# Kernel optimization log

Hardware: AMD Instinct MI355X
Metric: run time of the kernel (lower is better)

Reference implementation:

```python
import jax, jax.numpy as jnp
import numpy as np

B, H, L, D = 2, 8, 512, 64
TEMP = 8.0  # sqrt(D)


def setup_inputs() -> dict:
    key = jax.random.key(0)
    ks = jax.random.split(key, 6)
    q = jax.random.normal(ks[0], (B, H, L, D), jnp.float32)
    k = jax.random.normal(ks[1], (B, H, L, D), jnp.float32)
    v = jax.random.normal(ks[2], (B, H, L, D), jnp.float32)
    adj_k = jax.random.normal(ks[3], (B, L, L, D), jnp.float32)
    adj_v = jax.random.normal(ks[4], (B, L, L, D), jnp.float32)
    mask = jax.random.randint(ks[5], (B, 1, 1, L), 0, 2, jnp.int32)
    return {"q": q, "k": k, "v": v, "adj_k": adj_k, "adj_v": adj_v, "mask": mask}


def reference(q, k, v, adj_k, adj_v, mask):
    qs = q / TEMP
    # standard QK^T term + relation term: score[b,h,i,j] += q[b,h,i]. adj_k[b,i,j]
    attn = jnp.einsum('bhid,bhjd->bhij', qs, k) + jnp.einsum('bhid,bijd->bhij', qs, adj_k)
    attn = jnp.where(mask == 0, jnp.float32(-10000.0), attn)
    attn = jax.nn.softmax(attn, axis=-1)  # dropout p=0 (eval / deterministic)
    # standard AV term + relation term: out[b,h,i] += sum_j attn[b,h,i,j]*adj_v[b,i,j]
    out = jnp.einsum('bhij,bhjd->bhid', attn, v) + jnp.einsum('bhij,bijd->bhid', attn, adj_v)
    return out, attn
```

## Files before the change

kernel.cpp:

```cpp
#include <hip/hip_runtime.h>

constexpr int B  = 2;
constexpr int NH = 8;
constexpr int L  = 512;
constexpr int D  = 64;
constexpr float INV_TEMP = 0.125f;

__global__ __launch_bounds__(256) void k1_qk(const float* __restrict__ q,
                                             const float* __restrict__ k,
                                             float* __restrict__ s1) {
  const int bh = blockIdx.x, it = blockIdx.y, jt = blockIdx.z;
  __shared__ float Qs[64][68];
  __shared__ float Ks[128][68];
  const int t = threadIdx.x;
  const float* qb = q + ((size_t)bh * L + it * 64) * D;
  const float* kb = k + ((size_t)bh * L + jt * 128) * D;
#pragma unroll
  for (int n0 = 0; n0 < 4; ++n0) {
    int n = t + (n0 << 8);
    int r = n >> 4, c = (n & 15) << 2;
    float4 a = *(const float4*)(qb + (size_t)r * D + c);
    a.x *= INV_TEMP; a.y *= INV_TEMP; a.z *= INV_TEMP; a.w *= INV_TEMP;
    *(float4*)&Qs[r][c] = a;
  }
#pragma unroll
  for (int n0 = 0; n0 < 8; ++n0) {
    int n = t + (n0 << 8);
    int r = n >> 4, c = (n & 15) << 2;
    *(float4*)&Ks[r][c] = *(const float4*)(kb + (size_t)r * D + c);
  }
  __syncthreads();
  const int i0 = t >> 4, j0 = t & 15;
  float acc[4][8] = {};
#pragma unroll 1
  for (int kc = 0; kc < 64; kc += 4) {
    float4 a[4], b[8];
#pragma unroll
    for (int m = 0; m < 4; ++m) a[m] = *(const float4*)&Qs[i0 + 16 * m][kc];
#pragma unroll
    for (int n = 0; n < 8; ++n) b[n] = *(const float4*)&Ks[j0 + 16 * n][kc];
#pragma unroll
    for (int m = 0; m < 4; ++m)
#pragma unroll
      for (int n = 0; n < 8; ++n)
        acc[m][n] = fmaf(a[m].x, b[n].x,
                    fmaf(a[m].y, b[n].y,
                    fmaf(a[m].z, b[n].z,
                    fmaf(a[m].w, b[n].w, acc[m][n]))));
  }
  float* sb = s1 + ((size_t)bh * L + it * 64) * L + jt * 128;
#pragma unroll
  for (int m = 0; m < 4; ++m) {
    float* srow = sb + (size_t)(i0 + 16 * m) * L;
#pragma unroll
    for (int n = 0; n < 8; ++n) srow[j0 + 16 * n] = acc[m][n];
  }
}

__global__ __launch_bounds__(512, 8) void k2_fused(
    const float* __restrict__ q, const float* __restrict__ v,
    const float* __restrict__ adj_k, const float* __restrict__ adj_v,
    const int* __restrict__ mask, const float* __restrict__ s1,
    float* __restrict__ out, float* __restrict__ attn) {
  const int b = blockIdx.x >> 9, i = blockIdx.x & (L - 1);
  const int t = threadIdx.x;
  const int lane = t & 63;
  const int w = __builtin_amdgcn_readfirstlane(t >> 6);

  __shared__ float sc[NH][L];
  __shared__ float ak[64][65];

  const float* akb = adj_k + ((size_t)b * L + i) * (size_t)(L * D);
  const float* qh  = q  + (((size_t)b * NH + w) * L + i) * D;
  const float* s1r = s1 + (((size_t)b * NH + w) * L + i) * L;

  const int sr0 = t >> 4, scol = (t & 15) << 2, sr1 = sr0 + 32;
  float4 pf0 = *(const float4*)(akb + (size_t)sr0 * D + scol);
  float4 pf1 = *(const float4*)(akb + (size_t)sr1 * D + scol);

  for (int jc = 0; jc < L; jc += 64) {
    ak[sr0][scol] = pf0.x; ak[sr0][scol + 1] = pf0.y;
    ak[sr0][scol + 2] = pf0.z; ak[sr0][scol + 3] = pf0.w;
    ak[sr1][scol] = pf1.x; ak[sr1][scol + 1] = pf1.y;
    ak[sr1][scol + 2] = pf1.z; ak[sr1][scol + 3] = pf1.w;
    __syncthreads();
    if (jc + 64 < L) {
      const float* nb = akb + (size_t)(jc + 64) * D;
      pf0 = *(const float4*)(nb + (size_t)sr0 * D + scol);
      pf1 = *(const float4*)(nb + (size_t)sr1 * D + scol);
    }
    float acc = 0.f;
#pragma unroll
    for (int dc = 0; dc < D; dc += 4) {
      float4 q4 = *(const float4*)(qh + dc);
      acc = fmaf(q4.x, ak[lane][dc],
            fmaf(q4.y, ak[lane][dc + 1],
            fmaf(q4.z, ak[lane][dc + 2],
            fmaf(q4.w, ak[lane][dc + 3], acc))));
    }
    sc[w][jc + lane] = s1r[jc + lane] + acc * INV_TEMP;
    __syncthreads();
  }

  {
    const int* mrow = mask + b * L;
    float* arow = attn + (((size_t)b * NH + w) * L + i) * L;
    float vals[8];
    float mx = -3.4e38f;
#pragma unroll
    for (int m = 0; m < 8; ++m) {
      int jj = lane + (m << 6);
      float s = sc[w][jj];
      s = (mrow[jj] == 0) ? -10000.0f : s;
      vals[m] = s;
      mx = fmaxf(mx, s);
    }
#pragma unroll
    for (int off = 32; off > 0; off >>= 1) mx = fmaxf(mx, __shfl_xor(mx, off, 64));
    float sum = 0.f;
#pragma unroll
    for (int m = 0; m < 8; ++m) { vals[m] = __expf(vals[m] - mx); sum += vals[m]; }
#pragma unroll
    for (int off = 32; off > 0; off >>= 1) sum += __shfl_xor(sum, off, 64);
    const float inv = 1.0f / sum;
#pragma unroll
    for (int m = 0; m < 8; ++m) {
      int jj = lane + (m << 6);
      float p = vals[m] * inv;
      arow[jj] = p;
      sc[w][jj] = p;
    }
  }
  __syncthreads();

  {
    const int jb = w << 6;
    const float* avp = adj_v + ((size_t)b * L + i) * (size_t)(L * D)
                             + (size_t)jb * D + lane;
    const float* vb  = v + (size_t)b * NH * (size_t)(L * D)
                         + (size_t)jb * D + lane;
    float* opart = &ak[0][0];
#pragma unroll
    for (int g = 0; g < 2; ++g) {
      const int h0 = g * 4;
      float p0 = sc[h0][jb + lane],     p1 = sc[h0 + 1][jb + lane],
            p2 = sc[h0 + 2][jb + lane], p3 = sc[h0 + 3][jb + lane];
      const float* w0 = vb + (size_t)(h0    ) * (L * D);
      const float* w1 = vb + (size_t)(h0 + 1) * (L * D);
      const float* w2 = vb + (size_t)(h0 + 2) * (L * D);
      const float* w3 = vb + (size_t)(h0 + 3) * (L * D);
      float o0 = 0.f, o1 = 0.f, o2 = 0.f, o3 = 0.f;
#pragma unroll 4
      for (int j = 0; j < 64; ++j) {
        float av = avp[(size_t)j * D];
        float x0 = w0[(size_t)j * D];
        float x1 = w1[(size_t)j * D];
        float x2 = w2[(size_t)j * D];
        float x3 = w3[(size_t)j * D];
        float pj0 = __uint_as_float(__builtin_amdgcn_readlane(__float_as_uint(p0), j));
        float pj1 = __uint_as_float(__builtin_amdgcn_readlane(__float_as_uint(p1), j));
        float pj2 = __uint_as_float(__builtin_amdgcn_readlane(__float_as_uint(p2), j));
        float pj3 = __uint_as_float(__builtin_amdgcn_readlane(__float_as_uint(p3), j));
        o0 = fmaf(pj0, av + x0, o0);
        o1 = fmaf(pj1, av + x1, o1);
        o2 = fmaf(pj2, av + x2, o2);
        o3 = fmaf(pj3, av + x3, o3);
      }
      opart[(w << 9) + (h0    ) * 64 + lane] = o0;
      opart[(w << 9) + (h0 + 1) * 64 + lane] = o1;
      opart[(w << 9) + (h0 + 2) * 64 + lane] = o2;
      opart[(w << 9) + (h0 + 3) * 64 + lane] = o3;
    }
    __syncthreads();
    float r = 0.f;
#pragma unroll
    for (int wv = 0; wv < 8; ++wv) r += opart[(wv << 9) + (w << 6) + lane];
    out[(((size_t)b * NH + w) * L + i) * D + lane] = r;
  }
}

extern "C" void kernel_launch(void* const* d_in, const int* in_sizes, int n_in,
                              void* d_out, int out_size, void* d_ws, size_t ws_size,
                              hipStream_t stream) {
  const float* q     = (const float*)d_in[0];
  const float* k     = (const float*)d_in[1];
  const float* v     = (const float*)d_in[2];
  const float* adj_k = (const float*)d_in[3];
  const float* adj_v = (const float*)d_in[4];
  const int*   mask  = (const int*)d_in[5];
  float* out  = (float*)d_out;
  float* attn = out + (size_t)B * NH * L * D;
  float* s1   = (float*)d_ws;

  dim3 g1(B * NH, L / 64, L / 128);
  k1_qk<<<g1, 256, 0, stream>>>(q, k, s1);
  k2_fused<<<B * L, 512, 0, stream>>>(q, v, adj_k, adj_v, mask, s1, out, attn);
}
```

Measured before the change: 346.2 us.

## Split attn·V into separate tiled GEMM kernel and restructure adj_k/adj_v passes

The attn·V term is moved out of the fused per-row kernel into a new tiled GEMM kernel that reads attn back and adds its result into out. The fused kernel now handles only the adj_k score term and the adj_v output term. The adj_k pass reads each adjacency row once into registers and computes all heads together, with no shared-memory staging. The adj_v pass uses float4 loads and a shuffle reduction instead of per-head scalar strided loads of both v and adj_v. The QK kernel tile shrinks to 64x64 for more blocks, at the cost of a third launch and an extra round trip of attn through memory.

```diff
diff --git a/kernel.cpp b/kernel.cpp
--- a/kernel.cpp
+++ b/kernel.cpp
@@ -11,10 +11,10 @@
                                              float* __restrict__ s1) {
   const int bh = blockIdx.x, it = blockIdx.y, jt = blockIdx.z;
   __shared__ float Qs[64][68];
-  __shared__ float Ks[128][68];
+  __shared__ float Ks[64][68];
   const int t = threadIdx.x;
   const float* qb = q + ((size_t)bh * L + it * 64) * D;
-  const float* kb = k + ((size_t)bh * L + jt * 128) * D;
+  const float* kb = k + ((size_t)bh * L + jt * 64) * D;
 #pragma unroll
   for (int n0 = 0; n0 < 4; ++n0) {
     int n = t + (n0 << 8);
@@ -22,96 +22,86 @@
     float4 a = *(const float4*)(qb + (size_t)r * D + c);
     a.x *= INV_TEMP; a.y *= INV_TEMP; a.z *= INV_TEMP; a.w *= INV_TEMP;
     *(float4*)&Qs[r][c] = a;
-  }
-#pragma unroll
-  for (int n0 = 0; n0 < 8; ++n0) {
-    int n = t + (n0 << 8);
-    int r = n >> 4, c = (n & 15) << 2;
     *(float4*)&Ks[r][c] = *(const float4*)(kb + (size_t)r * D + c);
   }
   __syncthreads();
   const int i0 = t >> 4, j0 = t & 15;
-  float acc[4][8] = {};
+  float acc[4][4] = {};
 #pragma unroll 1
   for (int kc = 0; kc < 64; kc += 4) {
-    float4 a[4], b[8];
+    float4 a[4], b[4];
 #pragma unroll
     for (int m = 0; m < 4; ++m) a[m] = *(const float4*)&Qs[i0 + 16 * m][kc];
 #pragma unroll
-    for (int n = 0; n < 8; ++n) b[n] = *(const float4*)&Ks[j0 + 16 * n][kc];
+    for (int n = 0; n < 4; ++n) b[n] = *(const float4*)&Ks[j0 + 16 * n][kc];
 #pragma unroll
     for (int m = 0; m < 4; ++m)
 #pragma unroll
-      for (int n = 0; n < 8; ++n)
+      for (int n = 0; n < 4; ++n)
         acc[m][n] = fmaf(a[m].x, b[n].x,
                     fmaf(a[m].y, b[n].y,
                     fmaf(a[m].z, b[n].z,
                     fmaf(a[m].w, b[n].w, acc[m][n]))));
   }
-  float* sb = s1 + ((size_t)bh * L + it * 64) * L + jt * 128;
+  float* sb = s1 + ((size_t)bh * L + it * 64) * L + jt * 64;
 #pragma unroll
   for (int m = 0; m < 4; ++m) {
     float* srow = sb + (size_t)(i0 + 16 * m) * L;
 #pragma unroll
-    for (int n = 0; n < 8; ++n) srow[j0 + 16 * n] = acc[m][n];
-  }
-}
-
-__global__ __launch_bounds__(512, 8) void k2_fused(
-    const float* __restrict__ q, const float* __restrict__ v,
-    const float* __restrict__ adj_k, const float* __restrict__ adj_v,
-    const int* __restrict__ mask, const float* __restrict__ s1,
-    float* __restrict__ out, float* __restrict__ attn) {
+    for (int n = 0; n < 4; ++n) srow[j0 + 16 * n] = acc[m][n];
+  }
+}
+
+__global__ __launch_bounds__(512, 4) void k2_fused(
+    const float* __restrict__ q, const float* __restrict__ adj_k,
+    const float* __restrict__ adj_v, const int* __restrict__ mask,
+    const float* __restrict__ s1, float* __restrict__ out,
+    float* __restrict__ attn) {
   const int b = blockIdx.x >> 9, i = blockIdx.x & (L - 1);
   const int t = threadIdx.x;
   const int lane = t & 63;
   const int w = __builtin_amdgcn_readfirstlane(t >> 6);
-
+  const int jb = w << 6;
   __shared__ float sc[NH][L];
-  __shared__ float ak[64][65];
-
-  const float* akb = adj_k + ((size_t)b * L + i) * (size_t)(L * D);
-  const float* qh  = q  + (((size_t)b * NH + w) * L + i) * D;
-  const float* s1r = s1 + (((size_t)b * NH + w) * L + i) * L;
-
-  const int sr0 = t >> 4, scol = (t & 15) << 2, sr1 = sr0 + 32;
-  float4 pf0 = *(const float4*)(akb + (size_t)sr0 * D + scol);
-  float4 pf1 = *(const float4*)(akb + (size_t)sr1 * D + scol);
-
-  for (int jc = 0; jc < L; jc += 64) {
-    ak[sr0][scol] = pf0.x; ak[sr0][scol + 1] = pf0.y;
-    ak[sr0][scol + 2] = pf0.z; ak[sr0][scol + 3] = pf0.w;
-    ak[sr1][scol] = pf1.x; ak[sr1][scol + 1] = pf1.y;
-    ak[sr1][scol + 2] = pf1.z; ak[sr1][scol + 3] = pf1.w;
-    __syncthreads();
-    if (jc + 64 < L) {
-      const float* nb = akb + (size_t)(jc + 64) * D;
-      pf0 = *(const float4*)(nb + (size_t)sr0 * D + scol);
-      pf1 = *(const float4*)(nb + (size_t)sr1 * D + scol);
-    }
-    float acc = 0.f;
-#pragma unroll
-    for (int dc = 0; dc < D; dc += 4) {
-      float4 q4 = *(const float4*)(qh + dc);
-      acc = fmaf(q4.x, ak[lane][dc],
-            fmaf(q4.y, ak[lane][dc + 1],
-            fmaf(q4.z, ak[lane][dc + 2],
-            fmaf(q4.w, ak[lane][dc + 3], acc))));
-    }
-    sc[w][jc + lane] = s1r[jc + lane] + acc * INV_TEMP;
-    __syncthreads();
-  }
 
   {
-    const int* mrow = mask + b * L;
+    const float* akr = adj_k + (((size_t)b * L + i) * L + jb + lane) * D;
+    float4 row[16];
+#pragma unroll
+    for (int dc = 0; dc < 16; ++dc) row[dc] = *(const float4*)(akr + 4 * dc);
+    const int mv = mask[b * L + jb + lane];
+    float acc[NH];
+#pragma unroll
+    for (int h = 0; h < NH; ++h) {
+      const float* qh = q + (((size_t)b * NH + h) * L + i) * D;
+      float a0 = 0.f, a1 = 0.f;
+#pragma unroll
+      for (int dc = 0; dc < 16; dc += 2) {
+        float4 q4 = *(const float4*)(qh + 4 * dc);
+        float4 q5 = *(const float4*)(qh + 4 * dc + 4);
+        a0 = fmaf(q4.x, row[dc].x, fmaf(q4.y, row[dc].y,
+             fmaf(q4.z, row[dc].z, fmaf(q4.w, row[dc].w, a0))));
+        a1 = fmaf(q5.x, row[dc + 1].x, fmaf(q5.y, row[dc + 1].y,
+             fmaf(q5.z, row[dc + 1].z, fmaf(q5.w, row[dc + 1].w, a1))));
+      }
+      acc[h] = a0 + a1;
+    }
+#pragma unroll
+    for (int h = 0; h < NH; ++h) {
+      float s = s1[(((size_t)b * NH + h) * L + i) * L + jb + lane]
+                + acc[h] * INV_TEMP;
+      sc[h][jb + lane] = (mv == 0) ? -10000.0f : s;
+    }
+  }
+  __syncthreads();
+
+  {
     float* arow = attn + (((size_t)b * NH + w) * L + i) * L;
     float vals[8];
     float mx = -3.4e38f;
 #pragma unroll
     for (int m = 0; m < 8; ++m) {
-      int jj = lane + (m << 6);
-      float s = sc[w][jj];
-      s = (mrow[jj] == 0) ? -10000.0f : s;
+      float s = sc[w][lane + (m << 6)];
       vals[m] = s;
       mx = fmaxf(mx, s);
     }
@@ -134,49 +124,104 @@
   __syncthreads();
 
   {
-    const int jb = w << 6;
-    const float* avp = adj_v + ((size_t)b * L + i) * (size_t)(L * D)
-                             + (size_t)jb * D + lane;
-    const float* vb  = v + (size_t)b * NH * (size_t)(L * D)
-                         + (size_t)jb * D + lane;
-    float* opart = &ak[0][0];
-#pragma unroll
-    for (int g = 0; g < 2; ++g) {
-      const int h0 = g * 4;
-      float p0 = sc[h0][jb + lane],     p1 = sc[h0 + 1][jb + lane],
-            p2 = sc[h0 + 2][jb + lane], p3 = sc[h0 + 3][jb + lane];
-      const float* w0 = vb + (size_t)(h0    ) * (L * D);
-      const float* w1 = vb + (size_t)(h0 + 1) * (L * D);
-      const float* w2 = vb + (size_t)(h0 + 2) * (L * D);
-      const float* w3 = vb + (size_t)(h0 + 3) * (L * D);
-      float o0 = 0.f, o1 = 0.f, o2 = 0.f, o3 = 0.f;
+    const int js = lane >> 4, dq = lane & 15;
+    const float* avb = adj_v + ((size_t)b * L + i) * (size_t)(L * D)
+                             + (size_t)jb * D + 4 * dq;
+    float4 o[NH];
+#pragma unroll
+    for (int h = 0; h < NH; ++h) o[h] = make_float4(0.f, 0.f, 0.f, 0.f);
 #pragma unroll 4
-      for (int j = 0; j < 64; ++j) {
-        float av = avp[(size_t)j * D];
-        float x0 = w0[(size_t)j * D];
-        float x1 = w1[(size_t)j * D];
-        float x2 = w2[(size_t)j * D];
-        float x3 = w3[(size_t)j * D];
-        float pj0 = __uint_as_float(__builtin_amdgcn_readlane(__float_as_uint(p0), j));
-        float pj1 = __uint_as_float(__builtin_amdgcn_readlane(__float_as_uint(p1), j));
-        float pj2 = __uint_as_float(__builtin_amdgcn_readlane(__float_as_uint(p2), j));
-        float pj3 = __uint_as_float(__builtin_amdgcn_readlane(__float_as_uint(p3), j));
-        o0 = fmaf(pj0, av + x0, o0);
-        o1 = fmaf(pj1, av + x1, o1);
-        o2 = fmaf(pj2, av + x2, o2);
-        o3 = fmaf(pj3, av + x3, o3);
+    for (int jj = 0; jj < 64; jj += 4) {
+      const float4 av = *(const float4*)(avb + (size_t)(jj + js) * D);
+      const int j = jb + jj + js;
+#pragma unroll
+      for (int h = 0; h < NH; ++h) {
+        float p = sc[h][j];
+        o[h].x = fmaf(p, av.x, o[h].x);
+        o[h].y = fmaf(p, av.y, o[h].y);
+        o[h].z = fmaf(p, av.z, o[h].z);
+        o[h].w = fmaf(p, av.w, o[h].w);
       }
-      opart[(w << 9) + (h0    ) * 64 + lane] = o0;
-      opart[(w << 9) + (h0 + 1) * 64 + lane] = o1;
-      opart[(w << 9) + (h0 + 2) * 64 + lane] = o2;
-      opart[(w << 9) + (h0 + 3) * 64 + lane] = o3;
+    }
+#pragma unroll
+    for (int h = 0; h < NH; ++h) {
+      o[h].x += __shfl_xor(o[h].x, 16, 64); o[h].x += __shfl_xor(o[h].x, 32, 64);
+      o[h].y += __shfl_xor(o[h].y, 16, 64); o[h].y += __shfl_xor(o[h].y, 32, 64);
+      o[h].z += __shfl_xor(o[h].z, 16, 64); o[h].z += __shfl_xor(o[h].z, 32, 64);
+      o[h].w += __shfl_xor(o[h].w, 16, 64); o[h].w += __shfl_xor(o[h].w, 32, 64);
+    }
+    __syncthreads();
+    float* opart = &sc[0][0];
+    if (js == 0) {
+#pragma unroll
+      for (int h = 0; h < NH; ++h)
+        *(float4*)(opart + (((w << 3) + h) << 6) + 4 * dq) = o[h];
     }
     __syncthreads();
     float r = 0.f;
 #pragma unroll
-    for (int wv = 0; wv < 8; ++wv) r += opart[(wv << 9) + (w << 6) + lane];
+    for (int wv = 0; wv < 8; ++wv) r += opart[(((wv << 3) + w) << 6) + lane];
     out[(((size_t)b * NH + w) * L + i) * D + lane] = r;
   }
+}
+
+__global__ __launch_bounds__(256) void k3_av(const float* __restrict__ attn,
+                                             const float* __restrict__ v,
+                                             float* __restrict__ out) {
+  const int bh = blockIdx.x, it = blockIdx.y;
+  __shared__ float As[32][68];
+  __shared__ float Vt[64][65];
+  const int t = threadIdx.x;
+  const float* ab = attn + ((size_t)bh * L + it * 32) * L;
+  const float* vb = v + (size_t)bh * (size_t)(L * D);
+  const int i0 = t >> 4, j0 = t & 15;
+  float acc[2][4] = {};
+#pragma unroll 1
+  for (int jc = 0; jc < L; jc += 64) {
+    __syncthreads();
+#pragma unroll
+    for (int n0 = 0; n0 < 2; ++n0) {
+      int n = t + (n0 << 8);
+      int r = n >> 4, c = (n & 15) << 2;
+      *(float4*)&As[r][c] = *(const float4*)(ab + (size_t)r * L + jc + c);
+    }
+#pragma unroll
+    for (int n0 = 0; n0 < 4; ++n0) {
+      int n = t + (n0 << 8);
+      int r = n >> 4, c = (n & 15) << 2;
+      float4 a = *(const float4*)(vb + (size_t)(jc + r) * D + c);
+      Vt[c][r] = a.x; Vt[c + 1][r] = a.y; Vt[c + 2][r] = a.z; Vt[c + 3][r] = a.w;
+    }
+    __syncthreads();
+#pragma unroll 1
+    for (int kc = 0; kc < 64; kc += 4) {
+      float4 a[2];
+#pragma unroll
+      for (int m = 0; m < 2; ++m) a[m] = *(const float4*)&As[i0 + 16 * m][kc];
+      float bb[4][4];
+#pragma unroll
+      for (int n = 0; n < 4; ++n) {
+        const float* vr = &Vt[j0 + 16 * n][kc];
+        bb[n][0] = vr[0]; bb[n][1] = vr[1]; bb[n][2] = vr[2]; bb[n][3] = vr[3];
+      }
+#pragma unroll
+      for (int m = 0; m < 2; ++m)
+#pragma unroll
+        for (int n = 0; n < 4; ++n)
+          acc[m][n] = fmaf(a[m].x, bb[n][0],
+                      fmaf(a[m].y, bb[n][1],
+                      fmaf(a[m].z, bb[n][2],
+                      fmaf(a[m].w, bb[n][3], acc[m][n]))));
+    }
+  }
+  float* ob = out + ((size_t)bh * L + it * 32) * D;
+#pragma unroll
+  for (int m = 0; m < 2; ++m)
+#pragma unroll
+    for (int n = 0; n < 4; ++n) {
+      float* p = ob + (size_t)(i0 + 16 * m) * D + j0 + 16 * n;
+      *p += acc[m][n];
+    }
 }
 
 extern "C" void kernel_launch(void* const* d_in, const int* in_sizes, int n_in,
@@ -192,7 +237,9 @@
   float* attn = out + (size_t)B * NH * L * D;
   float* s1   = (float*)d_ws;
 
-  dim3 g1(B * NH, L / 64, L / 128);
+  dim3 g1(B * NH, L / 64, L / 64);
   k1_qk<<<g1, 256, 0, stream>>>(q, k, s1);
-  k2_fused<<<B * L, 512, 0, stream>>>(q, v, adj_k, adj_v, mask, s1, out, attn);
-}
+  k2_fused<<<B * L, 512, 0, stream>>>(q, adj_k, adj_v, mask, s1, out, attn);
+  dim3 g3(B * NH, L / 32);
+  k3_av<<<g3, 256, 0, stream>>>(attn, v, out);
+}
```

New measurement: 332.7 us. -3.9%, faster.
